# Optimization experiments

Measured on AMD Instinct MI355X. Metric: run time of the kernel, lower is better.

## Reference

```python
import jax, jax.numpy as jnp
import numpy as np

NUM_SHOT = 1024
D_MODEL = 512
NHEAD = 8
NLAYERS = 6
D_FF = 2048
EPS = 1e-5


def _ln(x, s, b):
    m = jnp.mean(x, axis=-1, keepdims=True)
    v = jnp.mean(jnp.square(x - m), axis=-1, keepdims=True)
    return (x - m) / jnp.sqrt(v + EPS) * s + b


def _mha(q_in, kv_in, w_qkv, b_qkv, w_o, b_o):
    # q_in: [Sq, D], kv_in: [Sk, D]; PyTorch in_proj layout [3D, D]
    D = q_in.shape[-1]
    hd = D // NHEAD
    wq, wk, wv = w_qkv[:D], w_qkv[D:2 * D], w_qkv[2 * D:]
    bq, bk, bv = b_qkv[:D], b_qkv[D:2 * D], b_qkv[2 * D:]
    q = (q_in @ wq.T + bq).reshape(-1, NHEAD, hd)
    k = (kv_in @ wk.T + bk).reshape(-1, NHEAD, hd)
    v = (kv_in @ wv.T + bv).reshape(-1, NHEAD, hd)
    scores = jnp.einsum('qhd,khd->hqk', q, k) * (1.0 / np.sqrt(hd))
    a = jax.nn.softmax(scores, axis=-1)
    o = jnp.einsum('hqk,khd->qhd', a, v).reshape(-1, D)
    return o @ w_o.T + b_o


def setup_inputs() -> dict:
    key = jax.random.key(0)
    ks = iter(jax.random.split(key, 40))
    L, D, F = NLAYERS, D_MODEL, D_FF
    SC = 0.05  # weight scale, keeps activations sane

    def w(shape):
        return jax.random.normal(next(ks), shape, dtype=jnp.float32) * SC

    inp = {'shot_feature': jax.random.normal(next(ks), (NUM_SHOT, D), dtype=jnp.float32)}
    inp.update(
        enc_qkv_w=w((L, 3 * D, D)), enc_qkv_b=jnp.zeros((L, 3 * D), jnp.float32),
        enc_out_w=w((L, D, D)), enc_out_b=jnp.zeros((L, D), jnp.float32),
        enc_ff1_w=w((L, F, D)), enc_ff1_b=jnp.zeros((L, F), jnp.float32),
        enc_ff2_w=w((L, D, F)), enc_ff2_b=jnp.zeros((L, D), jnp.float32),
        enc_ln1_s=jnp.ones((L, D), jnp.float32), enc_ln1_b=jnp.zeros((L, D), jnp.float32),
        enc_ln2_s=jnp.ones((L, D), jnp.float32), enc_ln2_b=jnp.zeros((L, D), jnp.float32),
        dec_sa_qkv_w=w((L, 3 * D, D)), dec_sa_qkv_b=jnp.zeros((L, 3 * D), jnp.float32),
        dec_sa_out_w=w((L, D, D)), dec_sa_out_b=jnp.zeros((L, D), jnp.float32),
        dec_ca_qkv_w=w((L, 3 * D, D)), dec_ca_qkv_b=jnp.zeros((L, 3 * D), jnp.float32),
        dec_ca_out_w=w((L, D, D)), dec_ca_out_b=jnp.zeros((L, D), jnp.float32),
        dec_ff1_w=w((L, F, D)), dec_ff1_b=jnp.zeros((L, F), jnp.float32),
        dec_ff2_w=w((L, D, F)), dec_ff2_b=jnp.zeros((L, D), jnp.float32),
        dec_ln1_s=jnp.ones((L, D), jnp.float32), dec_ln1_b=jnp.zeros((L, D), jnp.float32),
        dec_ln2_s=jnp.ones((L, D), jnp.float32), dec_ln2_b=jnp.zeros((L, D), jnp.float32),
        dec_ln3_s=jnp.ones((L, D), jnp.float32), dec_ln3_b=jnp.zeros((L, D), jnp.float32),
        enc_norm_s=jnp.ones((D,), jnp.float32), enc_norm_b=jnp.zeros((D,), jnp.float32),
        dec_norm_s=jnp.ones((D,), jnp.float32), dec_norm_b=jnp.zeros((D,), jnp.float32),
    )
    return inp


def reference(shot_feature, enc_qkv_w, enc_qkv_b, enc_out_w, enc_out_b,
              enc_ff1_w, enc_ff1_b, enc_ff2_w, enc_ff2_b,
              enc_ln1_s, enc_ln1_b, enc_ln2_s, enc_ln2_b,
              dec_sa_qkv_w, dec_sa_qkv_b, dec_sa_out_w, dec_sa_out_b,
              dec_ca_qkv_w, dec_ca_qkv_b, dec_ca_out_w, dec_ca_out_b,
              dec_ff1_w, dec_ff1_b, dec_ff2_w, dec_ff2_b,
              dec_ln1_s, dec_ln1_b, dec_ln2_s, dec_ln2_b, dec_ln3_s, dec_ln3_b,
              enc_norm_s, enc_norm_b, dec_norm_s, dec_norm_b):
    x = shot_feature.reshape(NUM_SHOT, D_MODEL)  # batch dim of 1 squeezed

    # --- encoder (post-LN, ReLU FFN, dropout=eval identity) ---
    mem = x
    for i in range(NLAYERS):
        a = _mha(mem, mem, enc_qkv_w[i], enc_qkv_b[i], enc_out_w[i], enc_out_b[i])
        mem = _ln(mem + a, enc_ln1_s[i], enc_ln1_b[i])
        f = jax.nn.relu(mem @ enc_ff1_w[i].T + enc_ff1_b[i]) @ enc_ff2_w[i].T + enc_ff2_b[i]
        mem = _ln(mem + f, enc_ln2_s[i], enc_ln2_b[i])
    mem = _ln(mem, enc_norm_s, enc_norm_b)

    # --- decoder (tgt == src, no masks, matching original usage) ---
    y = x
    for i in range(NLAYERS):
        a = _mha(y, y, dec_sa_qkv_w[i], dec_sa_qkv_b[i], dec_sa_out_w[i], dec_sa_out_b[i])
        y = _ln(y + a, dec_ln1_s[i], dec_ln1_b[i])
        a = _mha(y, mem, dec_ca_qkv_w[i], dec_ca_qkv_b[i], dec_ca_out_w[i], dec_ca_out_b[i])
        y = _ln(y + a, dec_ln2_s[i], dec_ln2_b[i])
        f = jax.nn.relu(y @ dec_ff1_w[i].T + dec_ff1_b[i]) @ dec_ff2_w[i].T + dec_ff2_b[i]
        y = _ln(y + f, dec_ln3_s[i], dec_ln3_b[i])
    attention_out = _ln(y, dec_norm_s, dec_norm_b)  # [S, D]

    # --- fused pairwise cosine similarity (replaces O(n^2) python loop) ---
    n = attention_out / jnp.linalg.norm(attention_out, axis=1, keepdims=True)
    final_result = jax.lax.stop_gradient(n @ n.T)  # .detach() in original
    return (final_result, attention_out)
```

## Files before the change

kernel.cpp:

```cpp
#include <hip/hip_runtime.h>


#define NLAY 6

typedef __attribute__((ext_vector_type(8))) short short8;
typedef __attribute__((ext_vector_type(4))) short short4v;
typedef __attribute__((ext_vector_type(4))) float f32x4;

typedef __attribute__((address_space(3))) short lds_short;
typedef __attribute__((address_space(1))) const unsigned short g_ushort;

__device__ __forceinline__ void gload16(const unsigned short* g, short* l) {
    __builtin_amdgcn_global_load_lds((g_ushort*)g, (lds_short*)l, 16, 0, 0);
}

__device__ __forceinline__ void waitvm(int n) {
    if (n == 0)       asm volatile("s_waitcnt vmcnt(0)" ::: "memory");
    else if (n == 4)  asm volatile("s_waitcnt vmcnt(4)" ::: "memory");
    else if (n == 8)  asm volatile("s_waitcnt vmcnt(8)" ::: "memory");
    else              asm volatile("s_waitcnt vmcnt(16)" ::: "memory");
}

__device__ inline unsigned short f2bu(float x) {
    unsigned u = __builtin_bit_cast(unsigned, x);
    unsigned r = (u + 0x7fffu + ((u >> 16) & 1u)) >> 16;
    return (unsigned short)r;
}

__device__ inline float b2f(unsigned short u) {
    return __builtin_bit_cast(float, (unsigned)u << 16);
}

struct WCvt {
    const float* src[10];
    unsigned short* dst[10];
    long cum[11];
};

__global__ __launch_bounds__(256)
void f2ball_k(WCvt wc)
{
    const long total = wc.cum[10];
    for (long c = (long)blockIdx.x * 256 + threadIdx.x; c < total;
         c += (long)gridDim.x * 256) {
        int t = 0;
        #pragma unroll
        for (int i = 1; i < 10; ++i) if (c >= wc.cum[i]) t = i;
        const long o = (c - wc.cum[t]) * 8;
        const float* s = wc.src[t];
        unsigned short* d = wc.dst[t];
        const float4 a = *(const float4*)(s + o);
        const float4 b = *(const float4*)(s + o + 4);
        short8 v;
        v[0] = (short)f2bu(a.x); v[1] = (short)f2bu(a.y);
        v[2] = (short)f2bu(a.z); v[3] = (short)f2bu(a.w);
        v[4] = (short)f2bu(b.x); v[5] = (short)f2bu(b.y);
        v[6] = (short)f2bu(b.z); v[7] = (short)f2bu(b.w);
        *(short8*)(d + o) = v;
    }
}

__global__ __launch_bounds__(256)
void f2b_k(const float* __restrict__ s, unsigned short* __restrict__ d, long n)
{
    const long stride = (long)gridDim.x * 256;
    for (long i = (long)blockIdx.x * 256 + threadIdx.x; i * 8 < n; i += stride) {
        const long o = i * 8;
        const float4 a = *(const float4*)(s + o);
        const float4 b = *(const float4*)(s + o + 4);
        short8 v;
        v[0] = (short)f2bu(a.x); v[1] = (short)f2bu(a.y);
        v[2] = (short)f2bu(a.z); v[3] = (short)f2bu(a.w);
        v[4] = (short)f2bu(b.x); v[5] = (short)f2bu(b.y);
        v[6] = (short)f2bu(b.z); v[7] = (short)f2bu(b.w);
        *(short8*)(d + o) = v;
    }
}

template<bool RELU, bool OBF16>
__global__ __launch_bounds__(256)
void gemm3_k(const unsigned short* __restrict__ A,
             const unsigned short* __restrict__ A2, int a2_col, int lda,
             const unsigned short* __restrict__ B, int ldb,
             const float* __restrict__ bias,
             void* __restrict__ Cv, int ldc, long sC,
             int K, float alpha,
             unsigned short* __restrict__ VTp, int vt_col0, int kz,
             long zB, int zBias, long zVT)
{
    __shared__ __align__(16) short As[3][4096];
    __shared__ __align__(16) short Bs[3][4096];
    const int bz = blockIdx.z;
    const int m0 = blockIdx.y * 64;
    const int n0 = blockIdx.x * 64;
    if (A2 && n0 >= a2_col) A = A2;
    A += (long)bz * kz;
    B += (long)bz * kz + (long)bz * zB;
    if (bias) bias += (long)bz * zBias;
    if (VTp)  VTp  += (long)bz * zVT;
    const int tid = threadIdx.x;
    const int w  = tid >> 6;
    const int l  = tid & 63;
    const int fr = l & 15;
    const int kc = l >> 4;

    f32x4 acc[4] = {};
    const int T = K >> 6;

    auto FILL = [&](int t, int buf) {
        const int k0 = t * 64;
        #pragma unroll
        for (int it = 0; it < 2; ++it) {
            const int row = w * 16 + it * 8 + (l >> 3);
            const int sl  = ((l & 7) ^ (row & 7)) * 8;
            gload16(A + (long)(m0 + row) * lda + k0 + sl, &As[buf][(w * 16 + it * 8) * 64]);
            gload16(B + (long)(n0 + row) * ldb + k0 + sl, &Bs[buf][(w * 16 + it * 8) * 64]);
        }
    };

    FILL(0, 0);
    if (T > 1) FILL(1, 1);
    for (int t = 0; t < T; ++t) {
        waitvm(t + 1 < T ? 4 : 0);
        __builtin_amdgcn_sched_barrier(0);
        __builtin_amdgcn_s_barrier();
        if (t + 2 < T) FILL(t + 2, (t + 2) % 3);
        const int cb = t % 3;
        #pragma unroll
        for (int ks = 0; ks < 2; ++ks) {
            const int arow = w * 16 + fr;
            const short8 af = *(const short8*)&As[cb][arow * 64 + (((ks * 4 + kc) ^ (arow & 7)) * 8)];
            #pragma unroll
            for (int c = 0; c < 4; ++c) {
                const int brow = c * 16 + fr;
                const short8 bf = *(const short8*)&Bs[cb][brow * 64 + (((ks * 4 + kc) ^ (brow & 7)) * 8)];
                acc[c] = __builtin_amdgcn_mfma_f32_16x16x32_bf16(af, bf, acc[c], 0, 0, 0);
            }
        }
    }

    #pragma unroll
    for (int c = 0; c < 4; ++c) {
        const int n = n0 + c * 16 + fr;
        const float bv = bias ? bias[n] : 0.0f;
        const bool do_vt = (VTp != nullptr) && (n >= vt_col0);
        #pragma unroll
        for (int i = 0; i < 4; ++i) {
            const long m = m0 + w * 16 + kc * 4 + i;
            float v = acc[c][i] * alpha + bv;
            if (RELU) v = fmaxf(v, 0.0f);
            if (OBF16) ((unsigned short*)Cv)[bz * sC + m * ldc + n] = f2bu(v);
            else       ((float*)Cv)[bz * sC + m * ldc + n] = v;
            if (do_vt) {
                const int vc = n - vt_col0;
                VTp[(long)(vc >> 6) * 65536 + (long)(vc & 63) * 1024 + m] = f2bu(v);
            }
        }
    }
}

__global__ __launch_bounds__(128)
void attnp_k(const unsigned short* __restrict__ Qb, int qld,
             const unsigned short* __restrict__ Kb, int kld,
             const unsigned short* __restrict__ VT,
             const unsigned short* __restrict__ wo,
             unsigned short* __restrict__ SLABb)
{
    __shared__ __align__(16) short U[36928];
    short* Ks = U;
    short* Vs = U + 16384;
    short* Ps = U + 32768;
    float* Of = (float*)(U + 34816);
    float* Ml = (float*)(U + 34816 + 2048);
    const int qt = blockIdx.x;
    const int h  = blockIdx.y;
    const int tid = threadIdx.x;
    const int w  = tid >> 6;
    const int l  = tid & 63;
    const int fr = l & 15;
    const int kc = l >> 4;

    const int qrow = qt * 16 + fr;
    short8 qf[2];
    qf[0] = *(const short8*)(Qb + (long)qrow * qld + h * 64 + kc * 8);
    qf[1] = *(const short8*)(Qb + (long)qrow * qld + h * 64 + 32 + kc * 8);

    auto FILL = [&](int t, int lbuf) {
        const int kb  = (w * 8 + t) * 64;
        const int buf = w * 2 + lbuf;
        #pragma unroll
        for (int it = 0; it < 8; ++it) {
            const int row = it * 8 + (l >> 3);
            const int sl  = ((l & 7) ^ (row & 7)) * 8;
            gload16(Kb + (long)(kb + row) * kld + h * 64 + sl, Ks + buf * 4096 + it * 512);
            gload16(VT + (long)h * 65536 + (long)row * 1024 + kb + sl, Vs + buf * 4096 + it * 512);
        }
    };

    float m_i[4], l_i[4];
    f32x4 acc_o[4] = {};
    #pragma unroll
    for (int i = 0; i < 4; ++i) { m_i[i] = -1e30f; l_i[i] = 0.f; }

    short* ps = Ps + w * 1024;

    FILL(0, 0); FILL(1, 1);
    for (int t = 0; t < 8; ++t) {
        waitvm(t == 7 ? 0 : 16);
        __builtin_amdgcn_sched_barrier(0);
        const int cb = w * 2 + (t & 1);

        f32x4 sacc[4] = {};
        #pragma unroll
        for (int ks = 0; ks < 2; ++ks) {
            #pragma unroll
            for (int c = 0; c < 4; ++c) {
                const int krow = c * 16 + fr;
                const short8 kf = *(const short8*)(Ks + cb * 4096 + krow * 64 + (((ks * 4 + kc) ^ (krow & 7)) * 8));
                sacc[c] = __builtin_amdgcn_mfma_f32_16x16x32_bf16(qf[ks], kf, sacc[c], 0, 0, 0);
            }
        }

        float p[4][4];
        #pragma unroll
        for (int i = 0; i < 4; ++i) {
            float tm = fmaxf(fmaxf(sacc[0][i], sacc[1][i]), fmaxf(sacc[2][i], sacc[3][i]));
            #pragma unroll
            for (int off = 8; off; off >>= 1) tm = fmaxf(tm, __shfl_xor(tm, off));
            tm *= 0.125f;
            const float mn = fmaxf(m_i[i], tm);
            const float sc = __expf(m_i[i] - mn);
            m_i[i] = mn;
            float ts = 0.f;
            #pragma unroll
            for (int c = 0; c < 4; ++c) { p[c][i] = __expf(sacc[c][i] * 0.125f - mn); ts += p[c][i]; }
            #pragma unroll
            for (int off = 8; off; off >>= 1) ts += __shfl_xor(ts, off);
            l_i[i] = l_i[i] * sc + ts;
            #pragma unroll
            for (int c = 0; c < 4; ++c) acc_o[c][i] *= sc;
        }

        #pragma unroll
        for (int c = 0; c < 4; ++c) {
            const int col = c * 16 + fr;
            #pragma unroll
            for (int i = 0; i < 4; ++i) {
                const int row = kc * 4 + i;
                ps[row * 64 + (((col >> 3) ^ (row & 7)) * 8) + (col & 7)] = (short)f2bu(p[c][i]);
            }
        }
        short8 pf[2];
        pf[0] = *(const short8*)(ps + fr * 64 + ((kc ^ (fr & 7)) * 8));
        pf[1] = *(const short8*)(ps + fr * 64 + (((4 + kc) ^ (fr & 7)) * 8));

        #pragma unroll
        for (int ks = 0; ks < 2; ++ks) {
            #pragma unroll
            for (int c = 0; c < 4; ++c) {
                const int drow = c * 16 + fr;
                const short8 vf = *(const short8*)(Vs + cb * 4096 + drow * 64 + (((ks * 4 + kc) ^ (drow & 7)) * 8));
                acc_o[c] = __builtin_amdgcn_mfma_f32_16x16x32_bf16(pf[ks], vf, acc_o[c], 0, 0, 0);
            }
        }
        if (t + 2 < 8) FILL(t + 2, t & 1);
    }

    if (w == 1) {
        #pragma unroll
        for (int c = 0; c < 4; ++c)
            #pragma unroll
            for (int i = 0; i < 4; ++i)
                Of[(kc * 4 + i) * 64 + c * 16 + fr] = acc_o[c][i];
        if (fr == 0) {
            #pragma unroll
            for (int i = 0; i < 4; ++i) {
                Ml[(kc * 4 + i) * 2]     = m_i[i];
                Ml[(kc * 4 + i) * 2 + 1] = l_i[i];
            }
        }
    }
    __syncthreads();
    short* po = Ps;
    if (w == 0) {
        #pragma unroll
        for (int i = 0; i < 4; ++i) {
            const int row = kc * 4 + i;
            const float m1 = Ml[row * 2], l1 = Ml[row * 2 + 1];
            const float M  = fmaxf(m_i[i], m1);
            const float e0 = __expf(m_i[i] - M);
            const float e1 = __expf(m1 - M);
            const float inv = 1.0f / (e0 * l_i[i] + e1 * l1);
            #pragma unroll
            for (int c = 0; c < 4; ++c) {
                const int col = c * 16 + fr;
                const float o = e0 * acc_o[c][i] + e1 * Of[row * 64 + col];
                po[row * 64 + (((col >> 3) ^ (row & 7)) * 8) + (col & 7)] = (short)f2bu(o * inv);
            }
        }
    }
    __syncthreads();

    unsigned short* SLABh = SLABb + (long)h * 524288;
    auto WSTAGE = [&](int c8, int lbuf) {
        const int n0c = c8 * 64;
        const int buf = w * 2 + lbuf;
        #pragma unroll
        for (int it = 0; it < 8; ++it) {
            const int row = it * 8 + (l >> 3);
            const int sl  = ((l & 7) ^ (row & 7)) * 8;
            gload16(wo + (long)(n0c + row) * 512 + h * 64 + sl, Ks + buf * 4096 + it * 512);
        }
    };

    WSTAGE(w * 4, 0);
    for (int j = 0; j < 4; ++j) {
        if (j + 1 < 4) WSTAGE(w * 4 + j + 1, (j + 1) & 1);
        waitvm(j + 1 < 4 ? 8 : 0);
        __builtin_amdgcn_sched_barrier(0);
        const int buf = w * 2 + (j & 1);
        f32x4 a2[4] = {};
        #pragma unroll
        for (int ks = 0; ks < 2; ++ks) {
            const int q = ks * 4 + kc;
            const short8 af = *(const short8*)(po + fr * 64 + ((q ^ (fr & 7)) * 8));
            #pragma unroll
            for (int ct = 0; ct < 4; ++ct) {
                const int brn = ct * 16 + fr;
                const short8 bf = *(const short8*)(Ks + buf * 4096 + brn * 64 + ((q ^ (brn & 7)) * 8));
                a2[ct] = __builtin_amdgcn_mfma_f32_16x16x32_bf16(af, bf, a2[ct], 0, 0, 0);
            }
        }
        const int c8 = w * 4 + j;
        #pragma unroll
        for (int ct = 0; ct < 4; ++ct) {
            const int n = c8 * 64 + ct * 16 + fr;
            #pragma unroll
            for (int i = 0; i < 4; ++i)
                SLABh[(long)(qt * 16 + kc * 4 + i) * 512 + n] = f2bu(a2[ct][i]);
        }
    }
}

template<int NSLAB, bool SB16>
__global__ __launch_bounds__(256)
void ln_k(const float* __restrict__ x, const void* __restrict__ slab,
          const float* __restrict__ bias,
          const float* __restrict__ s, const float* __restrict__ b,
          float* __restrict__ out, unsigned short* __restrict__ outb)
{
    const int lane = threadIdx.x & 63;
    const int row  = (blockIdx.x << 2) + (threadIdx.x >> 6);
    const float* px = x + (long)row * 512;
    float v[8];
    float sum = 0.f;
    #pragma unroll
    for (int i = 0; i < 8; ++i) {
        const int j = lane + (i << 6);
        v[i] = px[j];
        #pragma unroll
        for (int t = 0; t < NSLAB; ++t) {
            if (SB16) v[i] += b2f(((const unsigned short*)slab)[(long)t * 524288 + (long)row * 512 + j]);
            else      v[i] += ((const float*)slab)[(long)t * 524288 + (long)row * 512 + j];
        }
        if (NSLAB > 0) v[i] += bias[j];
        sum += v[i];
    }
    #pragma unroll
    for (int off = 32; off; off >>= 1) sum += __shfl_xor(sum, off);
    const float m = sum * (1.0f / 512.0f);
    float s2 = 0.f;
    #pragma unroll
    for (int i = 0; i < 8; ++i) { const float d = v[i] - m; s2 += d * d; }
    #pragma unroll
    for (int off = 32; off; off >>= 1) s2 += __shfl_xor(s2, off);
    const float inv = rsqrtf(s2 * (1.0f / 512.0f) + 1e-5f);
    #pragma unroll
    for (int i = 0; i < 8; ++i) {
        const int j = lane + (i << 6);
        const float r = (v[i] - m) * inv * s[j] + b[j];
        out[(long)row * 512 + j] = r;
        if (outb) outb[(long)row * 512 + j] = f2bu(r);
    }
}

__global__ __launch_bounds__(256)
void lnl2_k(const float* __restrict__ x,
            const float* __restrict__ s, const float* __restrict__ b,
            float* __restrict__ out_attn, unsigned short* __restrict__ nb)
{
    const int lane = threadIdx.x & 63;
    const int row  = (blockIdx.x << 2) + (threadIdx.x >> 6);
    const float* px = x + (long)row * 512;
    float v[8];
    float sum = 0.f;
    #pragma unroll
    for (int i = 0; i < 8; ++i) { v[i] = px[lane + (i << 6)]; sum += v[i]; }
    #pragma unroll
    for (int off = 32; off; off >>= 1) sum += __shfl_xor(sum, off);
    const float m = sum * (1.0f / 512.0f);
    float s2 = 0.f;
    #pragma unroll
    for (int i = 0; i < 8; ++i) { const float d = v[i] - m; s2 += d * d; }
    #pragma unroll
    for (int off = 32; off; off >>= 1) s2 += __shfl_xor(s2, off);
    const float inv = rsqrtf(s2 * (1.0f / 512.0f) + 1e-5f);
    float nrm = 0.f;
    #pragma unroll
    for (int i = 0; i < 8; ++i) {
        const int j = lane + (i << 6);
        v[i] = (v[i] - m) * inv * s[j] + b[j];
        out_attn[(long)row * 512 + j] = v[i];
        nrm += v[i] * v[i];
    }
    #pragma unroll
    for (int off = 32; off; off >>= 1) nrm += __shfl_xor(nrm, off);
    const float rinv = rsqrtf(nrm);
    #pragma unroll
    for (int i = 0; i < 8; ++i)
        nb[(long)row * 512 + lane + (i << 6)] = f2bu(v[i] * rinv);
}

__global__ __launch_bounds__(256)
void init_k(const float* __restrict__ x, float* __restrict__ mf, float* __restrict__ yf,
            unsigned short* __restrict__ mb, unsigned short* __restrict__ yb)
{
    const long i = ((long)blockIdx.x * 256 + threadIdx.x) * 4;
    const float4 v = *(const float4*)(x + i);
    *(float4*)(mf + i) = v;
    *(float4*)(yf + i) = v;
    short4v s;
    s[0] = (short)f2bu(v.x); s[1] = (short)f2bu(v.y);
    s[2] = (short)f2bu(v.z); s[3] = (short)f2bu(v.w);
    *(short4v*)(mb + i) = s;
    *(short4v*)(yb + i) = s;
}

static void gemm3(hipStream_t st, bool relu, bool obf16,
                  const unsigned short* A, int lda,
                  const unsigned short* B, int ldb,
                  const float* bias, void* C, int ldc, long sC,
                  int M, int N, int K, float alpha, int batch,
                  unsigned short* VTp = nullptr, int vt_col0 = 0,
                  const unsigned short* A2 = nullptr, int a2_col = 0,
                  int kz = 0, long zB = 0, int zBias = 0, long zVT = 0)
{
    dim3 g(N / 64, M / 64, batch);
    if (obf16) {
        if (relu) gemm3_k<true,  true ><<<g, 256, 0, st>>>(A, A2, a2_col, lda, B, ldb, bias, C, ldc, sC, K, alpha, VTp, vt_col0, kz, zB, zBias, zVT);
        else      gemm3_k<false, true ><<<g, 256, 0, st>>>(A, A2, a2_col, lda, B, ldb, bias, C, ldc, sC, K, alpha, VTp, vt_col0, kz, zB, zBias, zVT);
    } else {
        if (relu) gemm3_k<true,  false><<<g, 256, 0, st>>>(A, A2, a2_col, lda, B, ldb, bias, C, ldc, sC, K, alpha, VTp, vt_col0, kz, zB, zBias, zVT);
        else      gemm3_k<false, false><<<g, 256, 0, st>>>(A, A2, a2_col, lda, B, ldb, bias, C, ldc, sC, K, alpha, VTp, vt_col0, kz, zB, zBias, zVT);
    }
}

extern "C" void kernel_launch(void* const* d_in, const int* in_sizes, int n_in,
                              void* d_out, int out_size, void* d_ws, size_t ws_size,
                              hipStream_t stream)
{
    const float* x            = (const float*)d_in[0];
    const float* enc_qkv_w    = (const float*)d_in[1];
    const float* enc_qkv_b    = (const float*)d_in[2];
    const float* enc_out_w    = (const float*)d_in[3];
    const float* enc_out_b    = (const float*)d_in[4];
    const float* enc_ff1_w    = (const float*)d_in[5];
    const float* enc_ff1_b    = (const float*)d_in[6];
    const float* enc_ff2_w    = (const float*)d_in[7];
    const float* enc_ff2_b    = (const float*)d_in[8];
    const float* enc_ln1_s    = (const float*)d_in[9];
    const float* enc_ln1_b    = (const float*)d_in[10];
    const float* enc_ln2_s    = (const float*)d_in[11];
    const float* enc_ln2_b    = (const float*)d_in[12];
    const float* dec_sa_qkv_w = (const float*)d_in[13];
    const float* dec_sa_qkv_b = (const float*)d_in[14];
    const float* dec_sa_out_w = (const float*)d_in[15];
    const float* dec_sa_out_b = (const float*)d_in[16];
    const float* dec_ca_qkv_w = (const float*)d_in[17];
    const float* dec_ca_qkv_b = (const float*)d_in[18];
    const float* dec_ca_out_w = (const float*)d_in[19];
    const float* dec_ca_out_b = (const float*)d_in[20];
    const float* dec_ff1_w    = (const float*)d_in[21];
    const float* dec_ff1_b    = (const float*)d_in[22];
    const float* dec_ff2_w    = (const float*)d_in[23];
    const float* dec_ff2_b    = (const float*)d_in[24];
    const float* dec_ln1_s    = (const float*)d_in[25];
    const float* dec_ln1_b    = (const float*)d_in[26];
    const float* dec_ln2_s    = (const float*)d_in[27];
    const float* dec_ln2_b    = (const float*)d_in[28];
    const float* dec_ln3_s    = (const float*)d_in[29];
    const float* dec_ln3_b    = (const float*)d_in[30];
    const float* enc_norm_s   = (const float*)d_in[31];
    const float* enc_norm_b   = (const float*)d_in[32];
    const float* dec_norm_s   = (const float*)d_in[33];
    const float* dec_norm_b   = (const float*)d_in[34];

    char* p = (char*)d_ws;
    auto alloc = [&](size_t bytes) -> char* {
        char* r = p; p += (bytes + 255) & ~(size_t)255; return r;
    };
    float*          MEMf = (float*)alloc(1024 * 512 * 4);
    float*          Yf   = (float*)alloc(1024 * 512 * 4);
    unsigned short* MEMb = (unsigned short*)alloc(1024 * 512 * 2);
    unsigned short* Yb   = (unsigned short*)alloc(1024 * 512 * 2);
    unsigned short* QKVb = (unsigned short*)alloc(1024 * 1536 * 2);
    unsigned short* VT   = (unsigned short*)alloc(8L * 64 * 1024 * 2);
    char*           SLAB = alloc(8L * 1024 * 512 * 2);
    unsigned short* F1b  = (unsigned short*)alloc(1024L * 2048 * 2);
    unsigned short* NBb  = (unsigned short*)alloc(1024 * 512 * 2);
    unsigned short* QB   = (unsigned short*)alloc(1024 * 512 * 2);
    unsigned short* KVCA = (unsigned short*)alloc(6L * 1024 * 1024 * 2);
    unsigned short* VTCA = (unsigned short*)alloc(6L * 8 * 64 * 1024 * 2);

    const float* wsrc[10] = {enc_qkv_w, enc_out_w, enc_ff1_w, enc_ff2_w,
                             dec_sa_qkv_w, dec_sa_out_w, dec_ca_qkv_w, dec_ca_out_w,
                             dec_ff1_w, dec_ff2_w};
    const long wper[10] = {1536L*512, 512L*512, 2048L*512, 512L*2048,
                           1536L*512, 512L*512, 1536L*512, 512L*512,
                           2048L*512, 512L*2048};
    long wtot = 0;
    for (int t = 0; t < 10; ++t) wtot += wper[t] * NLAY;

    const size_t used = (size_t)(p - (char*)d_ws);
    const bool preconv = (ws_size > used) && ((ws_size - used) >= (size_t)wtot * 2 + 4096);

    unsigned short* wpre[10] = {};
    unsigned short* slots[2] = {};
    int slot_ctr = 0;
    if (preconv) {
        WCvt wc;
        wc.cum[0] = 0;
        for (int t = 0; t < 10; ++t) {
            wpre[t] = (unsigned short*)alloc((size_t)wper[t] * NLAY * 2);
            wc.src[t] = wsrc[t];
            wc.dst[t] = wpre[t];
            wc.cum[t + 1] = wc.cum[t] + wper[t] * NLAY / 8;
        }
        f2ball_k<<<dim3(2048), 256, 0, stream>>>(wc);
    } else {
        slots[0] = (unsigned short*)alloc(2048L * 512 * 2);
        slots[1] = (unsigned short*)alloc(2048L * 512 * 2);
    }
    auto W = [&](int t, int layer) -> const unsigned short* {
        if (preconv) return wpre[t] + (long)layer * wper[t];
        unsigned short* dst = slots[(slot_ctr++) & 1];
        const long n = wper[t];
        long blocks = (n / 8 + 255) / 256; if (blocks > 2048) blocks = 2048;
        f2b_k<<<dim3((unsigned)blocks), 256, 0, stream>>>(wsrc[t] + (long)layer * wper[t], dst, n);
        return dst;
    };

    float* out_gram = (float*)d_out;
    float* out_attn = out_gram + 1024 * 1024;

    auto run_self = [&](const unsigned short* xb_in, int wt_qkv, int wt_o, int layer,
                        const float* bqkv, const float* obias,
                        const float* lns, const float* lnb,
                        float* xf, unsigned short* xb) {
        gemm3(stream, false, true, xb_in, 512, W(wt_qkv, layer), 512, bqkv,
              QKVb, 1536, 0, 1024, 1536, 512, 1.0f, 1, VT, 1024);
        attnp_k<<<dim3(64, 8), 128, 0, stream>>>(QKVb, 1536, QKVb + 512, 1536, VT,
                                                 W(wt_o, layer), (unsigned short*)SLAB);
        ln_k<8, true><<<256, 256, 0, stream>>>(xf, SLAB, obias, lns, lnb, xf, xb);
    };
    auto run_ffn = [&](unsigned short* inb, int wt1, int wt2, int layer,
                       const float* b1, const float* f2bias,
                       const float* lns, const float* lnb,
                       float* xf, unsigned short* xb) {
        gemm3(stream, true, true, inb, 512, W(wt1, layer), 512, b1,
              F1b, 2048, 0, 1024, 2048, 512, 1.0f, 1);
        gemm3(stream, false, false, F1b, 2048, W(wt2, layer), 2048, nullptr,
              SLAB, 512, 524288, 1024, 512, 512, 1.0f, 4, nullptr, 0, nullptr, 0, 512);
        ln_k<4, false><<<256, 256, 0, stream>>>(xf, SLAB, f2bias, lns, lnb, xf, xb);
    };

    init_k<<<512, 256, 0, stream>>>(x, MEMf, Yf, MEMb, Yb);

    for (int i = 0; i < NLAY; ++i) {
        run_self(MEMb, 0, 1, i, enc_qkv_b + i * 1536, enc_out_b + i * 512,
                 enc_ln1_s + i * 512, enc_ln1_b + i * 512, MEMf, MEMb);
        run_ffn(MEMb, 2, 3, i, enc_ff1_b + i * 2048, enc_ff2_b + i * 512,
                enc_ln2_s + i * 512, enc_ln2_b + i * 512, MEMf, MEMb);
    }
    ln_k<0, false><<<256, 256, 0, stream>>>(MEMf, nullptr, nullptr, enc_norm_s, enc_norm_b, MEMf, MEMb);

    if (preconv) {
        gemm3(stream, false, true, MEMb, 512, wpre[6] + 512L * 512, 512,
              dec_ca_qkv_b + 512, KVCA, 1024, 1024L * 1024,
              1024, 1024, 512, 1.0f, 6, VTCA, 512,
              nullptr, 0, 0, 1536L * 512, 1536, 524288L);
    }

    for (int i = 0; i < NLAY; ++i) {
        run_self(Yb, 4, 5, i, dec_sa_qkv_b + i * 1536, dec_sa_out_b + i * 512,
                 dec_ln1_s + i * 512, dec_ln1_b + i * 512, Yf, Yb);

        if (preconv) {
            gemm3(stream, false, true, Yb, 512, W(6, i), 512, dec_ca_qkv_b + i * 1536,
                  QB, 512, 0, 1024, 512, 512, 1.0f, 1);
            attnp_k<<<dim3(64, 8), 128, 0, stream>>>(QB, 512,
                    KVCA + (long)i * 1024 * 1024, 1024, VTCA + (long)i * 524288,
                    W(7, i), (unsigned short*)SLAB);
        } else {
            gemm3(stream, false, true, Yb, 512, W(6, i), 512, dec_ca_qkv_b + i * 1536,
                  QKVb, 1536, 0, 1024, 1536, 512, 1.0f, 1, VT, 1024, MEMb, 512);
            attnp_k<<<dim3(64, 8), 128, 0, stream>>>(QKVb, 1536, QKVb + 512, 1536, VT,
                                                     W(7, i), (unsigned short*)SLAB);
        }
        ln_k<8, true><<<256, 256, 0, stream>>>(Yf, SLAB, dec_ca_out_b + i * 512,
                                               dec_ln2_s + i * 512, dec_ln2_b + i * 512, Yf, Yb);

        run_ffn(Yb, 8, 9, i, dec_ff1_b + i * 2048, dec_ff2_b + i * 512,
                dec_ln3_s + i * 512, dec_ln3_b + i * 512, Yf, Yb);
    }

    lnl2_k<<<256, 256, 0, stream>>>(Yf, dec_norm_s, dec_norm_b, out_attn, NBb);
    gemm3(stream, false, false, NBb, 512, NBb, 512, nullptr,
          out_gram, 1024, 0, 1024, 1024, 512, 1.0f, 1);
}
```

Baseline: 1.029 ms.

## Stage V-transpose through LDS, fuse final norms into LN, bf16 FFN slabs

The GEMM epilogue that wrote the transposed V copy with scattered per-element stores now stages the tile in shared memory and writes coalesced 16-byte rows. The encoder and decoder final LayerNorms (plus the row L2 normalisation) are folded into the last FFN LayerNorm kernel, which removes two launches and one activation round trip each. The FFN2 split-K partial slabs are now stored in bf16 instead of fp32, which halves slab traffic but adds rounding to the partial sums before the residual add.

```diff
diff --git a/kernel.cpp b/kernel.cpp
--- a/kernel.cpp
+++ b/kernel.cpp
@@ -143,7 +143,6 @@
     for (int c = 0; c < 4; ++c) {
         const int n = n0 + c * 16 + fr;
         const float bv = bias ? bias[n] : 0.0f;
-        const bool do_vt = (VTp != nullptr) && (n >= vt_col0);
         #pragma unroll
         for (int i = 0; i < 4; ++i) {
             const long m = m0 + w * 16 + kc * 4 + i;
@@ -151,11 +150,33 @@
             if (RELU) v = fmaxf(v, 0.0f);
             if (OBF16) ((unsigned short*)Cv)[bz * sC + m * ldc + n] = f2bu(v);
             else       ((float*)Cv)[bz * sC + m * ldc + n] = v;
-            if (do_vt) {
-                const int vc = n - vt_col0;
-                VTp[(long)(vc >> 6) * 65536 + (long)(vc & 63) * 1024 + m] = f2bu(v);
-            }
-        }
+        }
+    }
+
+    if (VTp != nullptr && n0 >= vt_col0) {
+        __syncthreads();
+        short* TB = &As[0][0];
+        #pragma unroll
+        for (int c = 0; c < 4; ++c) {
+            const int n = n0 + c * 16 + fr;
+            const float bv = bias ? bias[n] : 0.0f;
+            const int d = (n - vt_col0) & 63;
+            #pragma unroll
+            for (int i = 0; i < 4; ++i) {
+                float v = acc[c][i] * alpha + bv;
+                if (RELU) v = fmaxf(v, 0.0f);
+                TB[d * 72 + w * 16 + kc * 4 + i] = (short)f2bu(v);
+            }
+        }
+        __syncthreads();
+        const long hh = (long)((n0 - vt_col0) >> 6);
+        const int d  = tid >> 2;
+        const int mc = (tid & 3) * 16;
+        const short8 o0 = *(const short8*)&TB[d * 72 + mc];
+        const short8 o1 = *(const short8*)&TB[d * 72 + mc + 8];
+        unsigned short* dst = VTp + hh * 65536 + (long)d * 1024 + m0 + mc;
+        *(short8*)dst = o0;
+        *(short8*)(dst + 8) = o1;
     }
 }
 
@@ -342,12 +363,14 @@
     }
 }
 
-template<int NSLAB, bool SB16>
+template<int NSLAB, bool SB16, int FIN>
 __global__ __launch_bounds__(256)
 void ln_k(const float* __restrict__ x, const void* __restrict__ slab,
           const float* __restrict__ bias,
           const float* __restrict__ s, const float* __restrict__ b,
-          float* __restrict__ out, unsigned short* __restrict__ outb)
+          float* __restrict__ outf, unsigned short* __restrict__ outb,
+          const float* __restrict__ s2, const float* __restrict__ b2,
+          float* __restrict__ oattn, unsigned short* __restrict__ nbb)
 {
     const int lane = threadIdx.x & 63;
     const int row  = (blockIdx.x << 2) + (threadIdx.x >> 6);
@@ -369,56 +392,62 @@
     #pragma unroll
     for (int off = 32; off; off >>= 1) sum += __shfl_xor(sum, off);
     const float m = sum * (1.0f / 512.0f);
-    float s2 = 0.f;
+    float s2v = 0.f;
     #pragma unroll
-    for (int i = 0; i < 8; ++i) { const float d = v[i] - m; s2 += d * d; }
+    for (int i = 0; i < 8; ++i) { const float d = v[i] - m; s2v += d * d; }
     #pragma unroll
-    for (int off = 32; off; off >>= 1) s2 += __shfl_xor(s2, off);
-    const float inv = rsqrtf(s2 * (1.0f / 512.0f) + 1e-5f);
+    for (int off = 32; off; off >>= 1) s2v += __shfl_xor(s2v, off);
+    const float inv = rsqrtf(s2v * (1.0f / 512.0f) + 1e-5f);
+    float r[8];
     #pragma unroll
     for (int i = 0; i < 8; ++i) {
         const int j = lane + (i << 6);
-        const float r = (v[i] - m) * inv * s[j] + b[j];
-        out[(long)row * 512 + j] = r;
-        if (outb) outb[(long)row * 512 + j] = f2bu(r);
-    }
-}
-
-__global__ __launch_bounds__(256)
-void lnl2_k(const float* __restrict__ x,
-            const float* __restrict__ s, const float* __restrict__ b,
-            float* __restrict__ out_attn, unsigned short* __restrict__ nb)
-{
-    const int lane = threadIdx.x & 63;
-    const int row  = (blockIdx.x << 2) + (threadIdx.x >> 6);
-    const float* px = x + (long)row * 512;
-    float v[8];
-    float sum = 0.f;
-    #pragma unroll
-    for (int i = 0; i < 8; ++i) { v[i] = px[lane + (i << 6)]; sum += v[i]; }
-    #pragma unroll
-    for (int off = 32; off; off >>= 1) sum += __shfl_xor(sum, off);
-    const float m = sum * (1.0f / 512.0f);
-    float s2 = 0.f;
-    #pragma unroll
-    for (int i = 0; i < 8; ++i) { const float d = v[i] - m; s2 += d * d; }
-    #pragma unroll
-    for (int off = 32; off; off >>= 1) s2 += __shfl_xor(s2, off);
-    const float inv = rsqrtf(s2 * (1.0f / 512.0f) + 1e-5f);
-    float nrm = 0.f;
-    #pragma unroll
-    for (int i = 0; i < 8; ++i) {
-        const int j = lane + (i << 6);
-        v[i] = (v[i] - m) * inv * s[j] + b[j];
-        out_attn[(long)row * 512 + j] = v[i];
-        nrm += v[i] * v[i];
-    }
-    #pragma unroll
-    for (int off = 32; off; off >>= 1) nrm += __shfl_xor(nrm, off);
-    const float rinv = rsqrtf(nrm);
-    #pragma unroll
-    for (int i = 0; i < 8; ++i)
-        nb[(long)row * 512 + lane + (i << 6)] = f2bu(v[i] * rinv);
+        r[i] = (v[i] - m) * inv * s[j] + b[j];
+    }
+    if (FIN == 0) {
+        #pragma unroll
+        for (int i = 0; i < 8; ++i) {
+            const int j = lane + (i << 6);
+            outf[(long)row * 512 + j] = r[i];
+            outb[(long)row * 512 + j] = f2bu(r[i]);
+        }
+    } else {
+        float sum2 = 0.f;
+        #pragma unroll
+        for (int i = 0; i < 8; ++i) sum2 += r[i];
+        #pragma unroll
+        for (int off = 32; off; off >>= 1) sum2 += __shfl_xor(sum2, off);
+        const float m2 = sum2 * (1.0f / 512.0f);
+        float q2 = 0.f;
+        #pragma unroll
+        for (int i = 0; i < 8; ++i) { const float d = r[i] - m2; q2 += d * d; }
+        #pragma unroll
+        for (int off = 32; off; off >>= 1) q2 += __shfl_xor(q2, off);
+        const float inv2 = rsqrtf(q2 * (1.0f / 512.0f) + 1e-5f);
+        if (FIN == 1) {
+            #pragma unroll
+            for (int i = 0; i < 8; ++i) {
+                const int j = lane + (i << 6);
+                outb[(long)row * 512 + j] = f2bu((r[i] - m2) * inv2 * s2[j] + b2[j]);
+            }
+        } else {
+            float r2[8];
+            float nrm = 0.f;
+            #pragma unroll
+            for (int i = 0; i < 8; ++i) {
+                const int j = lane + (i << 6);
+                r2[i] = (r[i] - m2) * inv2 * s2[j] + b2[j];
+                oattn[(long)row * 512 + j] = r2[i];
+                nrm += r2[i] * r2[i];
+            }
+            #pragma unroll
+            for (int off = 32; off; off >>= 1) nrm += __shfl_xor(nrm, off);
+            const float rinv = rsqrtf(nrm);
+            #pragma unroll
+            for (int i = 0; i < 8; ++i)
+                nbb[(long)row * 512 + lane + (i << 6)] = f2bu(r2[i] * rinv);
+        }
+    }
 }
 
 __global__ __launch_bounds__(256)
@@ -561,17 +590,27 @@
               QKVb, 1536, 0, 1024, 1536, 512, 1.0f, 1, VT, 1024);
         attnp_k<<<dim3(64, 8), 128, 0, stream>>>(QKVb, 1536, QKVb + 512, 1536, VT,
                                                  W(wt_o, layer), (unsigned short*)SLAB);
-        ln_k<8, true><<<256, 256, 0, stream>>>(xf, SLAB, obias, lns, lnb, xf, xb);
+        ln_k<8, true, 0><<<256, 256, 0, stream>>>(xf, SLAB, obias, lns, lnb, xf, xb,
+                                                  nullptr, nullptr, nullptr, nullptr);
     };
     auto run_ffn = [&](unsigned short* inb, int wt1, int wt2, int layer,
                        const float* b1, const float* f2bias,
                        const float* lns, const float* lnb,
-                       float* xf, unsigned short* xb) {
+                       float* xf, unsigned short* xb, int fin,
+                       const float* s2, const float* b2) {
         gemm3(stream, true, true, inb, 512, W(wt1, layer), 512, b1,
               F1b, 2048, 0, 1024, 2048, 512, 1.0f, 1);
-        gemm3(stream, false, false, F1b, 2048, W(wt2, layer), 2048, nullptr,
+        gemm3(stream, false, true, F1b, 2048, W(wt2, layer), 2048, nullptr,
               SLAB, 512, 524288, 1024, 512, 512, 1.0f, 4, nullptr, 0, nullptr, 0, 512);
-        ln_k<4, false><<<256, 256, 0, stream>>>(xf, SLAB, f2bias, lns, lnb, xf, xb);
+        if (fin == 0)
+            ln_k<4, true, 0><<<256, 256, 0, stream>>>(xf, SLAB, f2bias, lns, lnb, xf, xb,
+                                                      nullptr, nullptr, nullptr, nullptr);
+        else if (fin == 1)
+            ln_k<4, true, 1><<<256, 256, 0, stream>>>(xf, SLAB, f2bias, lns, lnb, xf, xb,
+                                                      s2, b2, nullptr, nullptr);
+        else
+            ln_k<4, true, 2><<<256, 256, 0, stream>>>(xf, SLAB, f2bias, lns, lnb, xf, xb,
+                                                      s2, b2, out_attn, NBb);
     };
 
     init_k<<<512, 256, 0, stream>>>(x, MEMf, Yf, MEMb, Yb);
@@ -580,9 +619,9 @@
         run_self(MEMb, 0, 1, i, enc_qkv_b + i * 1536, enc_out_b + i * 512,
                  enc_ln1_s + i * 512, enc_ln1_b + i * 512, MEMf, MEMb);
         run_ffn(MEMb, 2, 3, i, enc_ff1_b + i * 2048, enc_ff2_b + i * 512,
-                enc_ln2_s + i * 512, enc_ln2_b + i * 512, MEMf, MEMb);
-    }
-    ln_k<0, false><<<256, 256, 0, stream>>>(MEMf, nullptr, nullptr, enc_norm_s, enc_norm_b, MEMf, MEMb);
+                enc_ln2_s + i * 512, enc_ln2_b + i * 512, MEMf, MEMb,
+                (i == NLAY - 1) ? 1 : 0, enc_norm_s, enc_norm_b);
+    }
 
     if (preconv) {
         gemm3(stream, false, true, MEMb, 512, wpre[6] + 512L * 512, 512,
@@ -607,14 +646,15 @@
             attnp_k<<<dim3(64, 8), 128, 0, stream>>>(QKVb, 1536, QKVb + 512, 1536, VT,
                                                      W(7, i), (unsigned short*)SLAB);
         }
-        ln_k<8, true><<<256, 256, 0, stream>>>(Yf, SLAB, dec_ca_out_b + i * 512,
-                                               dec_ln2_s + i * 512, dec_ln2_b + i * 512, Yf, Yb);
+        ln_k<8, true, 0><<<256, 256, 0, stream>>>(Yf, SLAB, dec_ca_out_b + i * 512,
+                                                  dec_ln2_s + i * 512, dec_ln2_b + i * 512,
+                                                  Yf, Yb, nullptr, nullptr, nullptr, nullptr);
 
         run_ffn(Yb, 8, 9, i, dec_ff1_b + i * 2048, dec_ff2_b + i * 512,
-                dec_ln3_s + i * 512, dec_ln3_b + i * 512, Yf, Yb);
-    }
-
-    lnl2_k<<<256, 256, 0, stream>>>(Yf, dec_norm_s, dec_norm_b, out_attn, NBb);
+                dec_ln3_s + i * 512, dec_ln3_b + i * 512, Yf, Yb,
+                (i == NLAY - 1) ? 2 : 0, dec_norm_s, dec_norm_b);
+    }
+
     gemm3(stream, false, false, NBb, 512, NBb, 512, nullptr,
           out_gram, 1024, 0, 1024, 1024, 512, 1.0f, 1);
 }
```

Result: faster. 960.1 us, median of 2 (-6.7%).
